# Kernel optimization log

Hardware: AMD Instinct MI355X
Metric: run time of the kernel (lower is better)

Reference implementation:

```python
import math
import jax, jax.numpy as jnp
import numpy as np

HIDDEN = 1024
HEADS = 16
HEAD = HIDDEN // HEADS
BUCKET = 32
MAXPOS = 512
REL = 2 * BUCKET - 1
EPS = 1e-7
L, B = 512, 16
STD = math.sqrt(2.0 / (5.0 * HIDDEN))


def _ln(x, g=None, b=None):
    m = x.mean(-1, keepdims=True)
    v = ((x - m) ** 2).mean(-1, keepdims=True)
    y = (x - m) * jax.lax.rsqrt(v + EPS)
    return y if g is None else y * g + b


def _bucket_indices(n):
    # DeBERTa-style log bucket relative positions, shifted to [0, 2*BUCKET-2]
    r = jnp.arange(n)[:, None] - jnp.arange(n)[None, :]
    mid = BUCKET // 2
    abs_pos = jnp.where((r < mid) & (r > -mid), mid - 1,
                        jnp.clip(jnp.abs(r), None, MAXPOS - 1))
    log_pos = jnp.ceil(jnp.log(abs_pos.astype(jnp.float32) / mid)
                       / math.log((MAXPOS - 1) / mid) * (mid - 1)).astype(jnp.int32) + mid
    bucket_pos = jnp.where(abs_pos <= mid, r, log_pos * jnp.sign(r))
    return (BUCKET - 1 + bucket_pos).astype(jnp.int32)


def setup_inputs() -> dict:
    key = jax.random.key(0)
    ks = jax.random.split(key, 8)
    return {
        'hidden_states': jax.random.normal(ks[0], (L, B, HIDDEN), jnp.float32),
        'attention_mask': jax.random.randint(ks[1], (B, 1, 1, L), 0, 2).astype(bool),
        'relative_embedding': jax.random.normal(ks[2], (REL, HIDDEN), jnp.float32),
        'wqk': jax.random.normal(ks[3], (2 * HIDDEN, HIDDEN), jnp.float32) * STD,
        'bqk': jnp.zeros((2 * HIDDEN,), jnp.float32),
        'wv': jax.random.normal(ks[4], (HIDDEN, HIDDEN), jnp.float32) * STD,
        'bv': jnp.zeros((HIDDEN,), jnp.float32),
        'wo': jax.random.normal(ks[5], (HIDDEN, HIDDEN), jnp.float32) * STD,
        'bo': jnp.zeros((HIDDEN,), jnp.float32),
        'ln_g': jnp.ones((HIDDEN,), jnp.float32),
        'ln_b': jnp.zeros((HIDDEN,), jnp.float32),
    }


def reference(hidden_states, attention_mask, relative_embedding,
              wqk, bqk, wv, bv, wo, bo, ln_g, ln_b):
    Lq, Bq, D = hidden_states.shape
    scale = 1.0 / math.sqrt(3 * HEAD)
    h = _ln(hidden_states)                                 # pre LN, no affine
    q, k = jnp.split(h @ wqk.T + bqk, 2, axis=-1)
    v = h @ wv.T + bv
    qpos, kpos = jnp.split(relative_embedding @ wqk.T + bqk, 2, axis=-1)
    qpos = qpos.reshape(REL, HEADS, HEAD)
    kpos = kpos.reshape(REL, HEADS, HEAD)
    # (L,B,D) -> (B,H,L,hd)
    qh = q.reshape(Lq, Bq, HEADS, HEAD).transpose(1, 2, 0, 3)
    kh = k.reshape(Lq, Bq, HEADS, HEAD).transpose(1, 2, 0, 3)
    vh = v.reshape(Lq, Bq, HEADS, HEAD).transpose(1, 2, 0, 3)
    scores = jnp.einsum('bhqd,bhkd->bhqk', qh, kh) * scale       # c2c
    qp = jnp.einsum('bhqd,khd->bhqk', qh, kpos) * scale          # c2p (k over buckets)
    pk = jnp.einsum('bhkd,qhd->bhqk', kh, qpos) * scale          # p2c (q over buckets)
    idx = jnp.broadcast_to(_bucket_indices(Lq), (Bq, HEADS, Lq, Lq))
    scores = scores + jnp.take_along_axis(qp, idx, axis=-1) \
                    + jnp.take_along_axis(pk, idx, axis=-2)
    # masked softmax: mask==True -> -inf before softmax, 0 after
    probs = jax.nn.softmax(jnp.where(attention_mask, -1e9, scores), axis=-1)
    probs = jnp.where(attention_mask, 0.0, probs)
    ctx = jnp.einsum('bhqk,bhkd->bhqd', probs, vh)
    ctx = ctx.transpose(2, 0, 1, 3).reshape(Lq, Bq, D)           # (L,B,D)
    out = ctx @ wo.T + bo
    return _ln(out, ln_g, ln_b)
```

## Files before the change

kernel.cpp:

```cpp
#include <hip/hip_runtime.h>
#include <hip/hip_bf16.h>

#define HID 1024
#define HEADS 16
#define HEAD 64
#define RELN 63
#define SEQ 512
#define BATCH 16
#define NROWS (SEQ*BATCH)
#define MEXT 8320
#define NQKV 3072
#define LNEPS 1e-7f
#define SCALEF 0.07216878364870323f

typedef __attribute__((ext_vector_type(4))) float  f32x4;
typedef __attribute__((ext_vector_type(8))) short  s16x8;
typedef __attribute__((ext_vector_type(4))) ushort u16x4;

static __device__ __forceinline__ ushort f2bf(float f) {
  union { float f; unsigned u; } v; v.f = f;
  unsigned r = v.u + 0x7fffu + ((v.u >> 16) & 1u);
  return (ushort)(r >> 16);
}
static __device__ __forceinline__ float bf2f(ushort u) {
  union { unsigned u; float f; } v; v.u = ((unsigned)u) << 16;
  return v.f;
}

__global__ void k_prep(const void* mask_raw, const float* bqk, const float* bv,
                       ushort* mask01, int* idx_tab, float* bcat) {
  __shared__ int s_isbool;
  int tid = threadIdx.x;
  if (tid == 0) s_isbool = 0;
  __syncthreads();
  const unsigned* mu = (const unsigned*)mask_raw;
  int bad = 0;
  for (int i = tid; i < 2048; i += 256) if (mu[i] > 1u) bad = 1;
  if (bad) s_isbool = 1;
  __syncthreads();
  int isbool = s_isbool;
  const unsigned char* m8 = (const unsigned char*)mask_raw;
  const int* m32 = (const int*)mask_raw;
  for (int i = tid; i < BATCH*SEQ; i += 256) {
    int m = isbool ? (int)m8[i] : m32[i];
    mask01[i] = m ? 1 : 0;
  }
  for (int i = tid; i < 1023; i += 256) {
    int r = i - 511;
    int a = r < 0 ? -r : r;
    int absp = (a < 16) ? 15 : (a < 511 ? a : 511);
    int idx;
    if (absp <= 16) idx = 31 + r;
    else {
      float v = logf((float)absp / 16.0f) / logf(511.0f / 16.0f) * 15.0f;
      int lp = (int)ceilf(v) + 16;
      idx = 31 + (r > 0 ? lp : -lp);
    }
    idx_tab[i] = idx;
  }
  for (int i = tid; i < 2048; i += 256) bcat[i] = bqk[i];
  for (int i = tid; i < 1024; i += 256) bcat[2048 + i] = bv[i];
}

__global__ void k_convert(const float* wqk, const float* wv, const float* wo,
                          ushort* wcat, ushort* wo_b) {
  int i = blockIdx.x * 256 + threadIdx.x;
  if (i < 2048 * 1024) wcat[i] = f2bf(wqk[i]);
  else if (i < 3072 * 1024) wcat[i] = f2bf(wv[i - 2048 * 1024]);
  if (i < 1024 * 1024) wo_b[i] = f2bf(wo[i]);
}

__global__ __launch_bounds__(256) void k_ln1(const float* hid, const float* rel, ushort* h_ext) {
  int row = blockIdx.x, tid = threadIdx.x;
  __shared__ float red[8];
  if (row < NROWS) {
    const float* src = hid + (size_t)row * HID;
    f32x4 x = *(const f32x4*)(src + tid * 4);
    float s = x[0] + x[1] + x[2] + x[3];
    #pragma unroll
    for (int m = 1; m < 64; m <<= 1) s += __shfl_xor(s, m);
    if ((tid & 63) == 0) red[tid >> 6] = s;
    __syncthreads();
    float mean = (red[0] + red[1] + red[2] + red[3]) * (1.0f / HID);
    float d0 = x[0] - mean, d1 = x[1] - mean, d2 = x[2] - mean, d3 = x[3] - mean;
    float sq = d0*d0 + d1*d1 + d2*d2 + d3*d3;
    #pragma unroll
    for (int m = 1; m < 64; m <<= 1) sq += __shfl_xor(sq, m);
    __syncthreads();
    if ((tid & 63) == 0) red[4 + (tid >> 6)] = sq;
    __syncthreads();
    float var = (red[4] + red[5] + red[6] + red[7]) * (1.0f / HID);
    float rs = rsqrtf(var + LNEPS);
    u16x4 o = { f2bf(d0*rs), f2bf(d1*rs), f2bf(d2*rs), f2bf(d3*rs) };
    *(u16x4*)(h_ext + (size_t)row * HID + tid * 4) = o;
  } else if (row < NROWS + RELN) {
    const float* src = rel + (size_t)(row - NROWS) * HID;
    f32x4 x = *(const f32x4*)(src + tid * 4);
    u16x4 o = { f2bf(x[0]), f2bf(x[1]), f2bf(x[2]), f2bf(x[3]) };
    *(u16x4*)(h_ext + (size_t)row * HID + tid * 4) = o;
  } else {
    u16x4 z = { 0, 0, 0, 0 };
    *(u16x4*)(h_ext + (size_t)row * HID + tid * 4) = z;
  }
}

template<int WRITE_F32>
__global__ __launch_bounds__(256) void k_gemm(const ushort* A, const ushort* Bw, const float* bias,
                                              ushort* Cb, float* Cf, int M, int N, int K) {
  __shared__ char smem[32768];
  char* As = smem;
  char* Bs = smem + 16384;
  int tid = threadIdx.x, lane = tid & 63, w = tid >> 6;
  int nbn = N >> 7;
  int per = gridDim.x >> 3;
  int gl = (blockIdx.x & 7) * per + (blockIdx.x >> 3);
  int bm = gl / nbn, bn = gl % nbn;
  int wr = w >> 1, wc = w & 1;
  int g = lane >> 4, r = lane & 15;
  f32x4 acc[4][4] = {};
  for (int ko = 0; ko < K; ko += 64) {
    __syncthreads();
    #pragma unroll
    for (int c = 0; c < 4; ++c) {
      int chunk = c * 256 + tid;
      int row = chunk >> 3;
      int kb = (chunk & 7) << 4;
      int kbs = kb ^ ((row & 7) << 4);
      const char* gA = (const char*)(A + (size_t)(bm * 128 + row) * K + ko) + kbs;
      const char* gB = (const char*)(Bw + (size_t)(bn * 128 + row) * K + ko) + kbs;
      __builtin_amdgcn_global_load_lds((const __attribute__((address_space(1))) void*)gA,
                                       (__attribute__((address_space(3))) void*)(As + c * 4096 + w * 1024),
                                       16, 0, 0);
      __builtin_amdgcn_global_load_lds((const __attribute__((address_space(1))) void*)gB,
                                       (__attribute__((address_space(3))) void*)(Bs + c * 4096 + w * 1024),
                                       16, 0, 0);
    }
    __syncthreads();
    #pragma unroll
    for (int kk = 0; kk < 2; ++kk) {
      s16x8 af[4], bf[4];
      #pragma unroll
      for (int mt = 0; mt < 4; ++mt) {
        int row = wr * 64 + mt * 16 + r;
        int kb = (kk * 64 + g * 16) ^ ((row & 7) << 4);
        af[mt] = *(const s16x8*)(As + row * 128 + kb);
      }
      #pragma unroll
      for (int nt = 0; nt < 4; ++nt) {
        int row = wc * 64 + nt * 16 + r;
        int kb = (kk * 64 + g * 16) ^ ((row & 7) << 4);
        bf[nt] = *(const s16x8*)(Bs + row * 128 + kb);
      }
      #pragma unroll
      for (int mt = 0; mt < 4; ++mt)
        #pragma unroll
        for (int nt = 0; nt < 4; ++nt)
          acc[mt][nt] = __builtin_amdgcn_mfma_f32_16x16x32_bf16(af[mt], bf[nt], acc[mt][nt], 0, 0, 0);
    }
  }
  #pragma unroll
  for (int nt = 0; nt < 4; ++nt) {
    int col = bn * 128 + wc * 64 + nt * 16 + r;
    float bvv = bias[col];
    #pragma unroll
    for (int mt = 0; mt < 4; ++mt) {
      int row0 = bm * 128 + wr * 64 + mt * 16 + g * 4;
      #pragma unroll
      for (int i = 0; i < 4; ++i) {
        float v = acc[mt][nt][i] + bvv;
        if (WRITE_F32) Cf[(size_t)(row0 + i) * N + col] = v;
        else           Cb[(size_t)(row0 + i) * N + col] = f2bf(v);
      }
    }
  }
}

__global__ __launch_bounds__(256) void k_pos(const ushort* qkv, const ushort* mask01,
                                             ushort* qp, ushort* pk) {
  int bh = blockIdx.x;
  int b = bh >> 4, h = bh & 15;
  int tid = threadIdx.x, lane = tid & 63, w = tid >> 6;
  int g = lane >> 4, r = lane & 15;
  __shared__ ushort mb[512];
  for (int i = tid; i < 512; i += 256) mb[i] = mask01[b * SEQ + i];
  __syncthreads();
  s16x8 bkp[4][2], bqp[4][2];
  #pragma unroll
  for (int nt = 0; nt < 4; ++nt)
    #pragma unroll
    for (int kk = 0; kk < 2; ++kk) {
      size_t rowp = (size_t)(NROWS + nt * 16 + r);
      int colq = h * 64 + kk * 32 + g * 8;
      bqp[nt][kk] = *(const s16x8*)(qkv + rowp * NQKV + colq);
      bkp[nt][kk] = *(const s16x8*)(qkv + rowp * NQKV + 1024 + colq);
    }
  for (int cc = 0; cc < 8; ++cc) {
    int rowbase = cc * 64 + w * 16;
    s16x8 aq[2], ak[2];
    #pragma unroll
    for (int kk = 0; kk < 2; ++kk) {
      size_t rowq = (size_t)((rowbase + r) * 16 + b);
      int colq = h * 64 + kk * 32 + g * 8;
      aq[kk] = *(const s16x8*)(qkv + rowq * NQKV + colq);
      ak[kk] = *(const s16x8*)(qkv + rowq * NQKV + 1024 + colq);
    }
    f32x4 accq[4] = {}, acck[4] = {};
    #pragma unroll
    for (int kk = 0; kk < 2; ++kk)
      #pragma unroll
      for (int nt = 0; nt < 4; ++nt) {
        accq[nt] = __builtin_amdgcn_mfma_f32_16x16x32_bf16(aq[kk], bkp[nt][kk], accq[nt], 0, 0, 0);
        acck[nt] = __builtin_amdgcn_mfma_f32_16x16x32_bf16(ak[kk], bqp[nt][kk], acck[nt], 0, 0, 0);
      }
    #pragma unroll
    for (int nt = 0; nt < 4; ++nt)
      #pragma unroll
      for (int i = 0; i < 4; ++i) {
        int q = rowbase + g * 4 + i;
        int t = nt * 16 + r;
        float biasv = mb[q] ? -1e9f : 0.0f;
        qp[(size_t)bh * SEQ * 64 + q * 64 + t] = f2bf(accq[nt][i] * SCALEF);
        pk[(size_t)bh * SEQ * 64 + q * 64 + t] = f2bf(acck[nt][i] * SCALEF + biasv);
      }
  }
}

__global__ __launch_bounds__(256) void k_vt(const ushort* qkv, ushort* vt, ushort* kc) {
  int bid = blockIdx.x;
  int bh = bid >> 3, lt = bid & 7;
  int b = bh >> 4, h = bh & 15;
  __shared__ ushort tile[64][72];
  int tid = threadIdx.x;
  #pragma unroll
  for (int c = 0; c < 2; ++c) {
    int e = (c * 256 + tid) * 8;
    int l = e >> 6, d0 = e & 63;
    size_t row = (size_t)((lt * 64 + l) * 16 + b);
    s16x8 kv = *(const s16x8*)(qkv + row * NQKV + 1024 + h * 64 + d0);
    #pragma unroll
    for (int j = 0; j < 8; ++j) kv[j] = (short)f2bf(bf2f((ushort)kv[j]) * SCALEF);
    *(s16x8*)(kc + ((size_t)bh * SEQ + lt * 64 + l) * 64 + d0) = kv;
    *(s16x8*)&tile[l][d0] = *(const s16x8*)(qkv + row * NQKV + 2048 + h * 64 + d0);
  }
  __syncthreads();
  #pragma unroll
  for (int c = 0; c < 2; ++c) {
    int e = (c * 256 + tid) * 8;
    int d = e >> 6, l0 = e & 63;
    ushort tmp[8];
    #pragma unroll
    for (int j = 0; j < 8; ++j) tmp[j] = tile[l0 + j][d];
    *(s16x8*)(vt + (size_t)(bh * 64 + d) * SEQ + lt * 64 + l0) = *(s16x8*)tmp;
  }
}

__global__ __launch_bounds__(256) void k_attn(const ushort* qkv, const ushort* qp_all, const ushort* pk_all,
                                              const ushort* kc, const ushort* vt,
                                              const int* idx_tab, ushort* ctx) {
  int bid = blockIdx.x;
  int slot = bid >> 3;
  int bh = (bid & 7) * 32 + (slot >> 3);
  int qt = slot & 7;
  int b = bh >> 4, h = bh & 15;
  int tid = threadIdx.x, lane = tid & 63, w = tid >> 6;
  int g = lane >> 4, r = lane & 15;

  __shared__ char   Ks[8192];
  __shared__ ushort qp_s[64][72];
  __shared__ ushort pk_s[64][72];
  __shared__ ushort p_s[4][16][72];
  __shared__ unsigned char idx_s[1024];

  const size_t qp_base = (size_t)bh * SEQ * 64 + (size_t)qt * 4096;
  const size_t pk_base = (size_t)bh * SEQ * 64;
  const char* kcb = (const char*)(kc + (size_t)bh * SEQ * 64);

  int krow = w * 8 + (lane >> 3);
  int ksrccol = ((lane & 7) ^ (lane >> 3)) << 4;

  #pragma unroll
  for (int c = 0; c < 2; ++c) {
    const char* src = kcb + (size_t)(c * 32 + krow) * 128 + ksrccol;
    __builtin_amdgcn_global_load_lds((const __attribute__((address_space(1))) void*)src,
                                     (__attribute__((address_space(3))) void*)(Ks + c * 4096 + w * 1024),
                                     16, 0, 0);
  }
  s16x8 pkreg[2];
  #pragma unroll
  for (int c = 0; c < 2; ++c)
    pkreg[c] = *(const s16x8*)(pk_all + pk_base + (size_t)(c * 256 + tid) * 8);
  #pragma unroll
  for (int c = 0; c < 2; ++c) {
    int chunk = c * 256 + tid;
    s16x8 v = *(const s16x8*)(qp_all + qp_base + (size_t)chunk * 8);
    *(s16x8*)&qp_s[chunk >> 3][(chunk & 7) * 8] = v;
  }
  for (int i = tid; i < 1023; i += 256) idx_s[i] = (unsigned char)idx_tab[i];
  s16x8 aq[2];
  int qg0 = qt * 64 + w * 16;
  #pragma unroll
  for (int kk = 0; kk < 2; ++kk) {
    size_t row = (size_t)((qg0 + r) * 16 + b);
    aq[kk] = *(const s16x8*)(qkv + row * NQKV + h * 64 + kk * 32 + g * 8);
  }
  #pragma unroll
  for (int c = 0; c < 2; ++c) {
    int chunk = c * 256 + tid;
    *(s16x8*)&pk_s[chunk >> 3][(chunk & 7) * 8] = pkreg[c];
  }
  __syncthreads();

  float m_i[4], l_i[4];
  f32x4 o_acc[4] = {};
  #pragma unroll
  for (int i = 0; i < 4; ++i) { m_i[i] = -3e38f; l_i[i] = 0.0f; }

  for (int kt = 0; kt < 8; ++kt) {
    if (kt < 7) {
      #pragma unroll
      for (int c = 0; c < 2; ++c)
        pkreg[c] = *(const s16x8*)(pk_all + pk_base + (size_t)(kt + 1) * 4096 + (size_t)(c * 256 + tid) * 8);
    }

    f32x4 s[4];
    #pragma unroll
    for (int nt = 0; nt < 4; ++nt) {
      f32x4 a = {};
      #pragma unroll
      for (int kk = 0; kk < 2; ++kk) {
        s16x8 bk = *(const s16x8*)(Ks + (nt * 16 + r) * 128 + ((kk * 64 + g * 16) ^ ((r & 7) << 4)));
        a = __builtin_amdgcn_mfma_f32_16x16x32_bf16(aq[kk], bk, a, 0, 0, 0);
      }
      s[nt] = a;
    }

    float tilemax[4];
    #pragma unroll
    for (int i = 0; i < 4; ++i) tilemax[i] = -3e38f;
    #pragma unroll
    for (int nt = 0; nt < 4; ++nt) {
      int kl = nt * 16 + r;
      int kgl = kt * 64 + kl;
      #pragma unroll
      for (int i = 0; i < 4; ++i) {
        int ql = w * 16 + g * 4 + i;
        int t = idx_s[(qt * 64 + ql) - kgl + 511];
        float v = s[nt][i] + bf2f(qp_s[ql][t]) + bf2f(pk_s[kl][t]);
        s[nt][i] = v;
        tilemax[i] = fmaxf(tilemax[i], v);
      }
    }
    __syncthreads();

    if (kt < 7) {
      #pragma unroll
      for (int c = 0; c < 2; ++c) {
        const char* src = kcb + (size_t)(kt + 1) * 8192 + (size_t)(c * 32 + krow) * 128 + ksrccol;
        __builtin_amdgcn_global_load_lds((const __attribute__((address_space(1))) void*)src,
                                         (__attribute__((address_space(3))) void*)(Ks + c * 4096 + w * 1024),
                                         16, 0, 0);
      }
      #pragma unroll
      for (int c = 0; c < 2; ++c) {
        int chunk = c * 256 + tid;
        *(s16x8*)&pk_s[chunk >> 3][(chunk & 7) * 8] = pkreg[c];
      }
    }
    s16x8 vreg[2][4];
    #pragma unroll
    for (int kk = 0; kk < 2; ++kk)
      #pragma unroll
      for (int nt = 0; nt < 4; ++nt)
        vreg[kk][nt] = *(const s16x8*)(vt + (size_t)(bh * 64 + nt * 16 + r) * SEQ + kt * 64 + kk * 32 + g * 8);

    #pragma unroll
    for (int i = 0; i < 4; ++i) {
      float v = tilemax[i];
      v = fmaxf(v, __shfl_xor(v, 1));
      v = fmaxf(v, __shfl_xor(v, 2));
      v = fmaxf(v, __shfl_xor(v, 4));
      v = fmaxf(v, __shfl_xor(v, 8));
      tilemax[i] = v;
    }
    float rs_i[4], psum[4];
    #pragma unroll
    for (int i = 0; i < 4; ++i) {
      float mnew = fmaxf(m_i[i], tilemax[i]);
      rs_i[i] = __expf(m_i[i] - mnew);
      m_i[i] = mnew;
      l_i[i] *= rs_i[i];
      psum[i] = 0.0f;
    }
    #pragma unroll
    for (int nt = 0; nt < 4; ++nt)
      #pragma unroll
      for (int i = 0; i < 4; ++i) {
        float pe = __expf(s[nt][i] - m_i[i]);
        psum[i] += pe;
        p_s[w][g * 4 + i][nt * 16 + r] = f2bf(pe);
      }
    #pragma unroll
    for (int i = 0; i < 4; ++i) {
      float v = psum[i];
      v += __shfl_xor(v, 1);
      v += __shfl_xor(v, 2);
      v += __shfl_xor(v, 4);
      v += __shfl_xor(v, 8);
      l_i[i] += v;
    }
    #pragma unroll
    for (int nt = 0; nt < 4; ++nt)
      #pragma unroll
      for (int i = 0; i < 4; ++i) o_acc[nt][i] *= rs_i[i];

    #pragma unroll
    for (int kk = 0; kk < 2; ++kk) {
      s16x8 pa = *(const s16x8*)&p_s[w][r][kk * 32 + g * 8];
      #pragma unroll
      for (int nt = 0; nt < 4; ++nt)
        o_acc[nt] = __builtin_amdgcn_mfma_f32_16x16x32_bf16(pa, vreg[kk][nt], o_acc[nt], 0, 0, 0);
    }

    if (kt < 7) __syncthreads();
  }

  #pragma unroll
  for (int i = 0; i < 4; ++i) {
    float inv = l_i[i] > 0.0f ? 1.0f / l_i[i] : 0.0f;
    int lq = qt * 64 + w * 16 + g * 4 + i;
    size_t rowc = (size_t)(lq * 16 + b);
    #pragma unroll
    for (int nt = 0; nt < 4; ++nt)
      ctx[rowc * HID + h * 64 + nt * 16 + r] = f2bf(o_acc[nt][i] * inv);
  }
}

__global__ __launch_bounds__(256) void k_ln2(const float* tmp, const float* gamma, const float* beta,
                                             float* out) {
  int row = blockIdx.x, tid = threadIdx.x;
  __shared__ float red[8];
  const float* src = tmp + (size_t)row * HID;
  f32x4 x = *(const f32x4*)(src + tid * 4);
  float s = x[0] + x[1] + x[2] + x[3];
  #pragma unroll
  for (int m = 1; m < 64; m <<= 1) s += __shfl_xor(s, m);
  if ((tid & 63) == 0) red[tid >> 6] = s;
  __syncthreads();
  float mean = (red[0] + red[1] + red[2] + red[3]) * (1.0f / HID);
  float d[4]; float sq = 0.0f;
  #pragma unroll
  for (int j = 0; j < 4; ++j) { d[j] = x[j] - mean; sq += d[j] * d[j]; }
  #pragma unroll
  for (int m = 1; m < 64; m <<= 1) sq += __shfl_xor(sq, m);
  __syncthreads();
  if ((tid & 63) == 0) red[4 + (tid >> 6)] = sq;
  __syncthreads();
  float var = (red[4] + red[5] + red[6] + red[7]) * (1.0f / HID);
  float rs = rsqrtf(var + LNEPS);
  f32x4 o;
  #pragma unroll
  for (int j = 0; j < 4; ++j) o[j] = d[j] * rs * gamma[tid * 4 + j] + beta[tid * 4 + j];
  *(f32x4*)(out + (size_t)row * HID + tid * 4) = o;
}

extern "C" void kernel_launch(void* const* d_in, const int* in_sizes, int n_in,
                              void* d_out, int out_size, void* d_ws, size_t ws_size,
                              hipStream_t stream) {
  (void)in_sizes; (void)n_in; (void)out_size; (void)ws_size;
  const float* hid  = (const float*)d_in[0];
  const void*  mask = d_in[1];
  const float* rel  = (const float*)d_in[2];
  const float* wqk  = (const float*)d_in[3];
  const float* bqk  = (const float*)d_in[4];
  const float* wv   = (const float*)d_in[5];
  const float* bv   = (const float*)d_in[6];
  const float* wo   = (const float*)d_in[7];
  const float* bo   = (const float*)d_in[8];
  const float* ln_g = (const float*)d_in[9];
  const float* ln_b = (const float*)d_in[10];

  char* ws = (char*)d_ws;
  ushort* wcat     = (ushort*)(ws);
  ushort* wo_b     = (ushort*)(ws + 6291456);
  float*  bcat     = (float*) (ws + 8388608);
  ushort* mask01   = (ushort*)(ws + 8400896);
  int*    idx_tab  = (int*)   (ws + 8433664);
  ushort* h_ext    = (ushort*)(ws + 8437760);
  ushort* qkv      = (ushort*)(ws + 25477120);
  ushort* qp_b     = (ushort*)(ws + 76595200);
  ushort* pk_b     = (ushort*)(ws + 93372416);
  ushort* vt       = (ushort*)(ws + 110149632);
  float*  tmp      = (float*) (ws + 126926848);
  ushort* ctx = h_ext;
  ushort* kc  = (ushort*)tmp;

  k_prep<<<1, 256, 0, stream>>>(mask, bqk, bv, mask01, idx_tab, bcat);
  k_convert<<<12288, 256, 0, stream>>>(wqk, wv, wo, wcat, wo_b);
  k_ln1<<<MEXT, 256, 0, stream>>>(hid, rel, h_ext);
  k_gemm<0><<<(MEXT / 128) * (NQKV / 128), 256, 0, stream>>>(h_ext, wcat, bcat, qkv, nullptr, MEXT, NQKV, 1024);
  k_pos<<<256, 256, 0, stream>>>(qkv, mask01, qp_b, pk_b);
  k_vt<<<2048, 256, 0, stream>>>(qkv, vt, kc);
  k_attn<<<2048, 256, 0, stream>>>(qkv, qp_b, pk_b, kc, vt, idx_tab, ctx);
  k_gemm<1><<<(NROWS / 128) * (1024 / 128), 256, 0, stream>>>(ctx, wo_b, bo, nullptr, tmp, NROWS, 1024, 1024);
  k_ln2<<<NROWS, 256, 0, stream>>>(tmp, ln_g, ln_b, (float*)d_out);
}
```

Measured before the change: 266.9 us.

## Restructure attention softmax with transposed scores, exp2, lazy rescale, and bf16 output projection

Folds log2(e) into the score scale so the softmax can use exp2. Swaps the MFMA operands so each lane owns one query row, which turns the per-row max and sum reductions into two cross-lane shuffles instead of four per row. Rescaling of the running output is skipped unless the max grows by more than a threshold. The output-projection GEMM now writes bf16 instead of fp32 before the final layer norm, which halves that traffic but loses precision before normalization.

```diff
diff --git a/kernel.cpp b/kernel.cpp
--- a/kernel.cpp
+++ b/kernel.cpp
@@ -11,7 +11,7 @@
 #define MEXT 8320
 #define NQKV 3072
 #define LNEPS 1e-7f
-#define SCALEF 0.07216878364870323f
+#define SCALE2 (0.07216878364870323f * 1.4426950408889634f)
 
 typedef __attribute__((ext_vector_type(4))) float  f32x4;
 typedef __attribute__((ext_vector_type(8))) short  s16x8;
@@ -219,8 +219,8 @@
         int q = rowbase + g * 4 + i;
         int t = nt * 16 + r;
         float biasv = mb[q] ? -1e9f : 0.0f;
-        qp[(size_t)bh * SEQ * 64 + q * 64 + t] = f2bf(accq[nt][i] * SCALEF);
-        pk[(size_t)bh * SEQ * 64 + q * 64 + t] = f2bf(acck[nt][i] * SCALEF + biasv);
+        qp[(size_t)bh * SEQ * 64 + q * 64 + t] = f2bf(accq[nt][i] * SCALE2);
+        pk[(size_t)bh * SEQ * 64 + q * 64 + t] = f2bf(acck[nt][i] * SCALE2 + biasv);
       }
   }
 }
@@ -238,7 +238,7 @@
     size_t row = (size_t)((lt * 64 + l) * 16 + b);
     s16x8 kv = *(const s16x8*)(qkv + row * NQKV + 1024 + h * 64 + d0);
     #pragma unroll
-    for (int j = 0; j < 8; ++j) kv[j] = (short)f2bf(bf2f((ushort)kv[j]) * SCALEF);
+    for (int j = 0; j < 8; ++j) kv[j] = (short)f2bf(bf2f((ushort)kv[j]) * SCALE2);
     *(s16x8*)(kc + ((size_t)bh * SEQ + lt * 64 + l) * 64 + d0) = kv;
     *(s16x8*)&tile[l][d0] = *(const s16x8*)(qkv + row * NQKV + 2048 + h * 64 + d0);
   }
@@ -310,10 +310,10 @@
   }
   __syncthreads();
 
-  float m_i[4], l_i[4];
+  float m_i = -3e38f, l_i = 0.0f;
   f32x4 o_acc[4] = {};
-  #pragma unroll
-  for (int i = 0; i < 4; ++i) { m_i[i] = -3e38f; l_i[i] = 0.0f; }
+  const ushort* qprow = &qp_s[w * 16 + r][0];
+  const int qglob511 = qt * 64 + w * 16 + r + 511;
 
   for (int kt = 0; kt < 8; ++kt) {
     if (kt < 7) {
@@ -329,25 +329,21 @@
       #pragma unroll
       for (int kk = 0; kk < 2; ++kk) {
         s16x8 bk = *(const s16x8*)(Ks + (nt * 16 + r) * 128 + ((kk * 64 + g * 16) ^ ((r & 7) << 4)));
-        a = __builtin_amdgcn_mfma_f32_16x16x32_bf16(aq[kk], bk, a, 0, 0, 0);
+        a = __builtin_amdgcn_mfma_f32_16x16x32_bf16(bk, aq[kk], a, 0, 0, 0);
       }
       s[nt] = a;
     }
 
-    float tilemax[4];
-    #pragma unroll
-    for (int i = 0; i < 4; ++i) tilemax[i] = -3e38f;
+    float m_loc = -3e38f;
     #pragma unroll
     for (int nt = 0; nt < 4; ++nt) {
-      int kl = nt * 16 + r;
-      int kgl = kt * 64 + kl;
       #pragma unroll
       for (int i = 0; i < 4; ++i) {
-        int ql = w * 16 + g * 4 + i;
-        int t = idx_s[(qt * 64 + ql) - kgl + 511];
-        float v = s[nt][i] + bf2f(qp_s[ql][t]) + bf2f(pk_s[kl][t]);
+        int kl = nt * 16 + g * 4 + i;
+        int t = idx_s[qglob511 - kt * 64 - kl];
+        float v = s[nt][i] + bf2f(qprow[t]) + bf2f(pk_s[kl][t]);
         s[nt][i] = v;
-        tilemax[i] = fmaxf(tilemax[i], v);
+        m_loc = fmaxf(m_loc, v);
       }
     }
     __syncthreads();
@@ -373,45 +369,38 @@
       for (int nt = 0; nt < 4; ++nt)
         vreg[kk][nt] = *(const s16x8*)(vt + (size_t)(bh * 64 + nt * 16 + r) * SEQ + kt * 64 + kk * 32 + g * 8);
 
-    #pragma unroll
-    for (int i = 0; i < 4; ++i) {
-      float v = tilemax[i];
-      v = fmaxf(v, __shfl_xor(v, 1));
-      v = fmaxf(v, __shfl_xor(v, 2));
-      v = fmaxf(v, __shfl_xor(v, 4));
-      v = fmaxf(v, __shfl_xor(v, 8));
-      tilemax[i] = v;
-    }
-    float rs_i[4], psum[4];
-    #pragma unroll
-    for (int i = 0; i < 4; ++i) {
-      float mnew = fmaxf(m_i[i], tilemax[i]);
-      rs_i[i] = __expf(m_i[i] - mnew);
-      m_i[i] = mnew;
-      l_i[i] *= rs_i[i];
-      psum[i] = 0.0f;
-    }
-    #pragma unroll
-    for (int nt = 0; nt < 4; ++nt)
+    float mx = fmaxf(m_loc, __shfl_xor(m_loc, 16));
+    mx = fmaxf(mx, __shfl_xor(mx, 32));
+
+    if (__any(mx > m_i + 8.0f)) {
+      float mnew = fmaxf(m_i, mx);
+      float rs = exp2f(m_i - mnew);
+      m_i = mnew;
+      l_i *= rs;
+      float rsb[4];
+      #pragma unroll
+      for (int i = 0; i < 4; ++i) rsb[i] = __shfl(rs, g * 4 + i);
+      #pragma unroll
+      for (int nt = 0; nt < 4; ++nt)
+        #pragma unroll
+        for (int i = 0; i < 4; ++i) o_acc[nt][i] *= rsb[i];
+    }
+
+    float psum = 0.0f;
+    #pragma unroll
+    for (int nt = 0; nt < 4; ++nt) {
+      u16x4 pk4;
       #pragma unroll
       for (int i = 0; i < 4; ++i) {
-        float pe = __expf(s[nt][i] - m_i[i]);
-        psum[i] += pe;
-        p_s[w][g * 4 + i][nt * 16 + r] = f2bf(pe);
-      }
-    #pragma unroll
-    for (int i = 0; i < 4; ++i) {
-      float v = psum[i];
-      v += __shfl_xor(v, 1);
-      v += __shfl_xor(v, 2);
-      v += __shfl_xor(v, 4);
-      v += __shfl_xor(v, 8);
-      l_i[i] += v;
-    }
-    #pragma unroll
-    for (int nt = 0; nt < 4; ++nt)
-      #pragma unroll
-      for (int i = 0; i < 4; ++i) o_acc[nt][i] *= rs_i[i];
+        float pe = exp2f(s[nt][i] - m_i);
+        psum += pe;
+        pk4[i] = f2bf(pe);
+      }
+      *(u16x4*)&p_s[w][r][nt * 16 + g * 4] = pk4;
+    }
+    psum += __shfl_xor(psum, 16);
+    psum += __shfl_xor(psum, 32);
+    l_i += psum;
 
     #pragma unroll
     for (int kk = 0; kk < 2; ++kk) {
@@ -424,9 +413,12 @@
     if (kt < 7) __syncthreads();
   }
 
+  float lb[4];
+  #pragma unroll
+  for (int i = 0; i < 4; ++i) lb[i] = __shfl(l_i, g * 4 + i);
   #pragma unroll
   for (int i = 0; i < 4; ++i) {
-    float inv = l_i[i] > 0.0f ? 1.0f / l_i[i] : 0.0f;
+    float inv = lb[i] > 0.0f ? 1.0f / lb[i] : 0.0f;
     int lq = qt * 64 + w * 16 + g * 4 + i;
     size_t rowc = (size_t)(lq * 16 + b);
     #pragma unroll
@@ -435,12 +427,12 @@
   }
 }
 
-__global__ __launch_bounds__(256) void k_ln2(const float* tmp, const float* gamma, const float* beta,
+__global__ __launch_bounds__(256) void k_ln2(const ushort* tmpb, const float* gamma, const float* beta,
                                              float* out) {
   int row = blockIdx.x, tid = threadIdx.x;
   __shared__ float red[8];
-  const float* src = tmp + (size_t)row * HID;
-  f32x4 x = *(const f32x4*)(src + tid * 4);
+  u16x4 xb = *(const u16x4*)(tmpb + (size_t)row * HID + tid * 4);
+  float x[4] = { bf2f(xb[0]), bf2f(xb[1]), bf2f(xb[2]), bf2f(xb[3]) };
   float s = x[0] + x[1] + x[2] + x[3];
   #pragma unroll
   for (int m = 1; m < 64; m <<= 1) s += __shfl_xor(s, m);
@@ -490,9 +482,10 @@
   ushort* qp_b     = (ushort*)(ws + 76595200);
   ushort* pk_b     = (ushort*)(ws + 93372416);
   ushort* vt       = (ushort*)(ws + 110149632);
-  float*  tmp      = (float*) (ws + 126926848);
+  char*   tmpr     = (ws + 126926848);
   ushort* ctx = h_ext;
-  ushort* kc  = (ushort*)tmp;
+  ushort* kc   = (ushort*)tmpr;
+  ushort* tmpb = (ushort*)tmpr;
 
   k_prep<<<1, 256, 0, stream>>>(mask, bqk, bv, mask01, idx_tab, bcat);
   k_convert<<<12288, 256, 0, stream>>>(wqk, wv, wo, wcat, wo_b);
@@ -501,6 +494,6 @@
   k_pos<<<256, 256, 0, stream>>>(qkv, mask01, qp_b, pk_b);
   k_vt<<<2048, 256, 0, stream>>>(qkv, vt, kc);
   k_attn<<<2048, 256, 0, stream>>>(qkv, qp_b, pk_b, kc, vt, idx_tab, ctx);
-  k_gemm<1><<<(NROWS / 128) * (1024 / 128), 256, 0, stream>>>(ctx, wo_b, bo, nullptr, tmp, NROWS, 1024, 1024);
-  k_ln2<<<NROWS, 256, 0, stream>>>(tmp, ln_g, ln_b, (float*)d_out);
-}
+  k_gemm<0><<<(NROWS / 128) * (1024 / 128), 256, 0, stream>>>(ctx, wo_b, bo, tmpb, nullptr, NROWS, 1024, 1024);
+  k_ln2<<<NROWS, 256, 0, stream>>>(tmpb, ln_g, ln_b, (float*)d_out);
+}
```

New measurement: 281.0 us. +5.3%, slower.
